# Optimization experiments

Measured on AMD Instinct MI355X. Metric: run time of the kernel, lower is better.

Reference implementation:

```python
import jax, jax.numpy as jnp
import numpy as np

Q_HEADS, KV_HEADS, D_K, D_V = 16, 4, 128, 128
GROUPS = Q_HEADS // KV_HEADS


def setup_inputs() -> dict:
    key = jax.random.key(0)
    ks = jax.random.split(key, 7)
    b, s, d = 2, 2048, 2048
    scale = 1.0 / np.sqrt(d).astype(np.float32)
    return {
        "Q": jax.random.normal(ks[0], (b, s, d), jnp.float32),
        "K": jax.random.normal(ks[1], (b, s, d), jnp.float32),
        "V": jax.random.normal(ks[2], (b, s, d), jnp.float32),
        "Wq": jax.random.normal(ks[3], (d, D_K * Q_HEADS), jnp.float32) * scale,
        "Wk": jax.random.normal(ks[4], (d, D_K * KV_HEADS), jnp.float32) * scale,
        "Wv": jax.random.normal(ks[5], (d, D_V * KV_HEADS), jnp.float32) * scale,
        "Wo": jax.random.normal(ks[6], (D_V * KV_HEADS, d), jnp.float32) * scale,
    }


def reference(Q, K, V, Wq, Wk, Wv, Wo):
    b, lq, _ = Q.shape
    lk = K.shape[1]
    # projections -> (b, heads, len, d)
    q = (Q @ Wq).reshape(b, lq, Q_HEADS, D_K).transpose(0, 2, 1, 3)
    k = (K @ Wk).reshape(b, lk, KV_HEADS, D_K).transpose(0, 2, 1, 3)
    v = (V @ Wv).reshape(b, lk, KV_HEADS, D_V).transpose(0, 2, 1, 3)
    # GQA quirk: scores summed over group dim g before softmax
    qr = q.reshape(b, GROUPS, KV_HEADS, lq, D_K)
    scores = jnp.einsum('bghqd,bhkd->bhqk', qr, k) / jnp.asarray(D_K ** 0.5, q.dtype)
    causal = jnp.tril(jnp.ones((lq, lk), bool))
    scores = jnp.where(causal[None, None], scores, jnp.asarray(-1e9, scores.dtype))
    attn = jax.nn.softmax(scores, axis=-1)  # (b, kv_heads, lq, lk)
    out = jnp.einsum('bhqk,bhkd->bhqd', attn, v)  # (b, kv_heads, lq, d_v)
    out = out.transpose(0, 2, 1, 3).reshape(b, lq, KV_HEADS * D_V)
    return out @ Wo
```

## Files before the change

### kernel.cpp

```cpp
#include <hip/hip_runtime.h>
#include <hip/hip_bf16.h>

typedef __attribute__((ext_vector_type(8))) short short8;
typedef __attribute__((ext_vector_type(4))) float f32x4;

#define MFMA16 __builtin_amdgcn_mfma_f32_16x16x32_bf16

__device__ inline unsigned short f2bf(float f) {
  __hip_bfloat16 h = __float2bfloat16(f);
  unsigned short u;
  __builtin_memcpy(&u, &h, 2);
  return u;
}

__device__ inline float bf2f(unsigned short u) {
  unsigned int x = ((unsigned int)u) << 16;
  float f;
  __builtin_memcpy(&f, &x, 4);
  return f;
}

__device__ inline void storeC(unsigned short* p, float v) { *p = f2bf(v); }
__device__ inline void storeC(float* p, float v) { *p = v; }

__device__ inline void gload16(const void* g, void* l) {
  __builtin_amdgcn_global_load_lds(
      (const __attribute__((address_space(1))) unsigned int*)g,
      (__attribute__((address_space(3))) unsigned int*)l,
      16, 0, 0);
}

__global__ __launch_bounds__(256)
void wqsum_t(const float* __restrict__ wq, unsigned short* __restrict__ dst) {
  __shared__ float t[64][65];
  const int n0 = blockIdx.x * 64, d0 = blockIdx.y * 64;
  const int tid = threadIdx.x;
#pragma unroll
  for (int it = 0; it < 16; ++it) {
    const int idx = it * 256 + tid;
    const int dd = idx >> 6, nn = idx & 63;
    const float* p = wq + (size_t)(d0 + dd) * 2048 + n0 + nn;
    t[dd][nn] = p[0] + p[512] + p[1024] + p[1536];
  }
  __syncthreads();
#pragma unroll
  for (int it = 0; it < 16; ++it) {
    const int idx = it * 256 + tid;
    const int nn = idx >> 6, dd = idx & 63;
    dst[(size_t)(n0 + nn) * 2048 + d0 + dd] = f2bf(t[dd][nn]);
  }
}

__global__ __launch_bounds__(256)
void transpose_w(const float* __restrict__ src, unsigned short* __restrict__ dst,
                 int R, int C) {
  __shared__ float t[64][65];
  const int c0 = blockIdx.x * 64, r0 = blockIdx.y * 64;
  const int tid = threadIdx.x;
#pragma unroll
  for (int it = 0; it < 16; ++it) {
    const int idx = it * 256 + tid;
    const int r = idx >> 6, c = idx & 63;
    t[r][c] = src[(size_t)(r0 + r) * C + c0 + c];
  }
  __syncthreads();
#pragma unroll
  for (int it = 0; it < 16; ++it) {
    const int idx = it * 256 + tid;
    const int rr = idx >> 6, cc = idx & 63;
    dst[(size_t)(c0 + rr) * R + r0 + cc] = f2bf(t[cc][rr]);
  }
}

__global__ __launch_bounds__(256)
void vtrans(const unsigned short* __restrict__ vh, unsigned short* __restrict__ vt) {
  __shared__ unsigned short t[64][72];
  const int s0 = blockIdx.x * 64;
  const int d0 = blockIdx.y * 64;
  const int bh = blockIdx.z;
  const int brow = (bh >> 2) * 2048;
  const int h = bh & 3;
  const int tid = threadIdx.x;
#pragma unroll
  for (int it = 0; it < 2; ++it) {
    const int idx = it * 256 + tid;
    const int s = idx >> 3;
    const int dd = (idx & 7) << 3;
    *(short8*)&t[s][dd] =
        *(const short8*)(vh + (size_t)(brow + s0 + s) * 512 + h * 128 + d0 + dd);
  }
  __syncthreads();
#pragma unroll
  for (int it = 0; it < 2; ++it) {
    const int idx = it * 256 + tid;
    const int dd = idx >> 3;
    const int ss = (idx & 7) << 3;
    short8 o;
#pragma unroll
    for (int e = 0; e < 8; ++e) o[e] = (short)t[ss + e][dd];
    *(short8*)(vt + ((size_t)bh * 128 + d0 + dd) * 2048 + s0 + ss) = o;
  }
}

template <bool AF32, typename CT, int KS>
__global__ __launch_bounds__(256)
void gemm_bt(const void* A0, const void* A1, const void* A2,
             const unsigned short* __restrict__ Bt, CT* __restrict__ C,
             int K, int N, size_t sB, size_t sC) {
  __shared__ unsigned short As[128 * 64];
  __shared__ unsigned short Bs[128 * 64];

  const int tid = threadIdx.x;
  const int lane = tid & 63;
  const int wv = tid >> 6;
  const int wm = (wv >> 1) << 6;
  const int wn = (wv & 1) << 6;
  const int l15 = lane & 15;
  const int l4 = lane >> 4;
  const int lsw = (l15 & 7) << 4;

  const int nwg = gridDim.x;
  const int bid = blockIdx.x;
  const int job = (bid & 7) * (nwg >> 3) + (bid >> 3);
  const int ntile = N >> 7;
  const int per_ks = nwg / KS;
  const int ks = (KS > 1) ? (job / per_ks) : 0;
  const int jj = job - ks * per_ks;
  const int z = jj / (32 * ntile);
  const int rem = jj - z * 32 * ntile;
  const int m0 = (rem / ntile) << 7;
  const int n0 = (rem % ntile) << 7;
  const int kbeg = ks * (K / KS);
  const int kend = kbeg + K / KS;

  const void* Az = (z == 0) ? A0 : (z == 1) ? A1 : A2;
  const unsigned short* Ab = (const unsigned short*)Az;
  const float* Af = (const float*)Az;
  const unsigned short* Bz = Bt + sB * (size_t)z;

  const f32x4 zero = {0.f, 0.f, 0.f, 0.f};
  f32x4 acc[4][4];
#pragma unroll
  for (int i = 0; i < 4; ++i)
#pragma unroll
    for (int j = 0; j < 4; ++j) acc[i][j] = zero;

  const int srow = tid >> 3;
  const int scol = (tid & 7) << 3;
  const int scolsw = scol ^ ((srow & 7) << 3);

  float4 ar[8];

  auto issueB = [&](int k0) {
#pragma unroll
    for (int s = 0; s < 4; ++s) {
      const unsigned short* bsrc =
          Bz + (size_t)(n0 + srow + s * 32) * K + k0 + scolsw;
      gload16(bsrc, (char*)Bs + tid * 16 + s * 4096);
    }
  };
  auto issueA16 = [&](int k0) {
#pragma unroll
    for (int s = 0; s < 4; ++s) {
      const unsigned short* asrc =
          Ab + (size_t)(m0 + srow + s * 32) * K + k0 + scolsw;
      gload16(asrc, (char*)As + tid * 16 + s * 4096);
    }
  };
  auto loadA = [&](int k0) {
#pragma unroll
    for (int s = 0; s < 4; ++s) {
      const float* asrc = Af + (size_t)(m0 + srow + s * 32) * K + k0 + scol;
      ar[2 * s] = *(const float4*)(asrc);
      ar[2 * s + 1] = *(const float4*)(asrc + 4);
    }
  };
  auto writeA = [&]() {
#pragma unroll
    for (int s = 0; s < 4; ++s) {
      short8 o;
      o[0] = (short)f2bf(ar[2 * s].x); o[1] = (short)f2bf(ar[2 * s].y);
      o[2] = (short)f2bf(ar[2 * s].z); o[3] = (short)f2bf(ar[2 * s].w);
      o[4] = (short)f2bf(ar[2 * s + 1].x); o[5] = (short)f2bf(ar[2 * s + 1].y);
      o[6] = (short)f2bf(ar[2 * s + 1].z); o[7] = (short)f2bf(ar[2 * s + 1].w);
      *(short8*)((char*)As + (srow + s * 32) * 128 + scolsw * 2) = o;
    }
  };

  if constexpr (AF32) loadA(kbeg);

  for (int k0 = kbeg; k0 < kend; k0 += 64) {
    if constexpr (AF32) writeA(); else issueA16(k0);
    issueB(k0);
    if constexpr (AF32) {
      if (k0 + 64 < kend) loadA(k0 + 64);
    }
    __syncthreads();
#pragma unroll
    for (int kk = 0; kk < 2; ++kk) {
      const int kb = (kk * 64 + (l4 << 4)) ^ lsw;
      short8 a[4], b[4];
#pragma unroll
      for (int i = 0; i < 4; ++i)
        a[i] = *(const short8*)((const char*)As + (wm + i * 16 + l15) * 128 + kb);
#pragma unroll
      for (int j = 0; j < 4; ++j)
        b[j] = *(const short8*)((const char*)Bs + (wn + j * 16 + l15) * 128 + kb);
#pragma unroll
      for (int i = 0; i < 4; ++i)
#pragma unroll
        for (int j = 0; j < 4; ++j)
          acc[i][j] = MFMA16(a[i], b[j], acc[i][j], 0, 0, 0);
    }
    __syncthreads();
  }

  CT* Cz = C + sC * (size_t)(ks * 3 + z);
#pragma unroll
  for (int i = 0; i < 4; ++i) {
    const int row0 = m0 + wm + i * 16 + (l4 << 2);
#pragma unroll
    for (int j = 0; j < 4; ++j) {
      const int col = n0 + wn + j * 16 + l15;
#pragma unroll
      for (int r = 0; r < 4; ++r)
        storeC(&Cz[(size_t)(row0 + r) * N + col], acc[i][j][r]);
    }
  }
}

__global__ __launch_bounds__(256)
void qkv_combine(const unsigned short* __restrict__ pC,
                 unsigned short* __restrict__ dst) {
  const size_t HALF = 6291456;
  size_t i = ((size_t)blockIdx.x * 256 + threadIdx.x) * 8;
  const size_t stride = (size_t)gridDim.x * 256 * 8;
  for (; i < HALF; i += stride) {
    const short8 a = *(const short8*)(pC + i);
    const short8 b = *(const short8*)(pC + HALF + i);
    short8 o;
#pragma unroll
    for (int e = 0; e < 8; ++e)
      o[e] = (short)f2bf(bf2f((unsigned short)a[e]) + bf2f((unsigned short)b[e]));
    *(short8*)(dst + i) = o;
  }
}

__global__ __launch_bounds__(128)
void attn_split(const unsigned short* __restrict__ qh,
                const unsigned short* __restrict__ kh,
                const unsigned short* __restrict__ vt,
                unsigned short* __restrict__ Oh,
                unsigned short* __restrict__ pO,
                float* __restrict__ pml) {
  __shared__ unsigned short P_lds[2][32][36];
  const int tid = threadIdx.x;
  const int lane = tid & 63;
  const int wave = tid >> 6;
  const int l15 = lane & 15;
  const int l4 = lane >> 4;
  const int bh = blockIdx.y;
  const int brow = (bh >> 2) * 2048;
  const int h = bh & 3;

  int j = blockIdx.x, g = 0;
  while (j >= 2 * (g + 1) * (g + 2)) ++g;
  const int rem = j - 2 * g * (g + 1);
  const int r_ = rem / (g + 1);
  const int c_ = rem - r_ * (g + 1);
  const int qt = 4 * g + r_;
  const int k_begin = c_ << 8;
  const int k_end = (c_ == g) ? (qt + 1) * 64 : ((c_ + 1) << 8);
  const int qrow_w = qt * 64 + wave * 32;
  const float SCALE = 0.08838834764831845f;

  short8 qf[2][4];
#pragma unroll
  for (int m = 0; m < 2; ++m) {
    const unsigned short* qp =
        qh + (size_t)(brow + qrow_w + m * 16 + l15) * 512 + h * 128 + (l4 << 3);
#pragma unroll
    for (int kk = 0; kk < 4; ++kk) qf[m][kk] = *(const short8*)(qp + kk * 32);
  }

  const f32x4 zero = {0.f, 0.f, 0.f, 0.f};
  f32x4 o_acc[2][8];
#pragma unroll
  for (int m = 0; m < 2; ++m)
#pragma unroll
    for (int i = 0; i < 8; ++i) o_acc[m][i] = zero;
  float m_run[2][4], l_run[2][4];
#pragma unroll
  for (int m = 0; m < 2; ++m)
#pragma unroll
    for (int r = 0; r < 4; ++r) { m_run[m][r] = -1e30f; l_run[m][r] = 0.f; }

  const int nt = (k_end - k_begin) >> 5;
  for (int t = 0; t < nt; ++t) {
    const int kbase = k_begin + t * 32;
    f32x4 sa[2][2];
    sa[0][0] = zero; sa[0][1] = zero; sa[1][0] = zero; sa[1][1] = zero;
#pragma unroll
    for (int n = 0; n < 2; ++n) {
      short8 kf[4];
      const unsigned short* kp =
          kh + (size_t)(brow + kbase + n * 16 + l15) * 512 + h * 128 + (l4 << 3);
#pragma unroll
      for (int kk = 0; kk < 4; ++kk) kf[kk] = *(const short8*)(kp + kk * 32);
#pragma unroll
      for (int kk = 0; kk < 4; ++kk) {
        sa[0][n] = MFMA16(qf[0][kk], kf[kk], sa[0][n], 0, 0, 0);
        sa[1][n] = MFMA16(qf[1][kk], kf[kk], sa[1][n], 0, 0, 0);
      }
    }
    const bool need_mask = (kbase + 31 > qrow_w);
    float p[2][2][4];
#pragma unroll
    for (int m = 0; m < 2; ++m)
#pragma unroll
      for (int n = 0; n < 2; ++n)
#pragma unroll
        for (int r = 0; r < 4; ++r) {
          float v = sa[m][n][r] * SCALE;
          if (need_mask) {
            const int kc = kbase + n * 16 + l15;
            const int qr = qrow_w + m * 16 + (l4 << 2) + r;
            if (kc > qr) v = -1e30f;
          }
          p[m][n][r] = v;
        }
    float alpha[2][4];
#pragma unroll
    for (int m = 0; m < 2; ++m)
#pragma unroll
      for (int r = 0; r < 4; ++r) {
        float tmax = fmaxf(p[m][0][r], p[m][1][r]);
#pragma unroll
        for (int o = 1; o <= 8; o <<= 1) tmax = fmaxf(tmax, __shfl_xor(tmax, o));
        const float mn = fmaxf(m_run[m][r], tmax);
        alpha[m][r] = __expf(m_run[m][r] - mn);
        m_run[m][r] = mn;
      }
#pragma unroll
    for (int m = 0; m < 2; ++m)
#pragma unroll
      for (int r = 0; r < 4; ++r) {
        p[m][0][r] = __expf(p[m][0][r] - m_run[m][r]);
        p[m][1][r] = __expf(p[m][1][r] - m_run[m][r]);
        float s = p[m][0][r] + p[m][1][r];
#pragma unroll
        for (int o = 1; o <= 8; o <<= 1) s += __shfl_xor(s, o);
        l_run[m][r] = l_run[m][r] * alpha[m][r] + s;
      }
#pragma unroll
    for (int m = 0; m < 2; ++m)
#pragma unroll
      for (int d8 = 0; d8 < 8; ++d8)
#pragma unroll
        for (int r = 0; r < 4; ++r) o_acc[m][d8][r] *= alpha[m][r];
#pragma unroll
    for (int m = 0; m < 2; ++m)
#pragma unroll
      for (int n = 0; n < 2; ++n)
#pragma unroll
        for (int r = 0; r < 4; ++r)
          P_lds[wave][m * 16 + (l4 << 2) + r][n * 16 + l15] = f2bf(p[m][n][r]);
    short8 pa[2];
#pragma unroll
    for (int m = 0; m < 2; ++m)
      pa[m] = *(const short8*)((const char*)&P_lds[wave][0][0] +
                               (m * 16 + l15) * 72 + (l4 << 4));
#pragma unroll
    for (int d8 = 0; d8 < 8; ++d8) {
      const short8 vb = *(const short8*)(
          vt + ((size_t)bh * 128 + d8 * 16 + l15) * 2048 + kbase + (l4 << 3));
      o_acc[0][d8] = MFMA16(pa[0], vb, o_acc[0][d8], 0, 0, 0);
      o_acc[1][d8] = MFMA16(pa[1], vb, o_acc[1][d8], 0, 0, 0);
    }
  }

  if (g == 0) {
#pragma unroll
    for (int m = 0; m < 2; ++m)
#pragma unroll
      for (int d8 = 0; d8 < 8; ++d8)
#pragma unroll
        for (int r = 0; r < 4; ++r) {
          const int row = brow + qrow_w + m * 16 + (l4 << 2) + r;
          Oh[(size_t)row * 512 + h * 128 + d8 * 16 + l15] =
              f2bf(o_acc[m][d8][r] / l_run[m][r]);
        }
  } else {
    const int slot = bh * 144 + blockIdx.x;
    unsigned short* po = pO + (size_t)slot * 64 * 128;
#pragma unroll
    for (int m = 0; m < 2; ++m)
#pragma unroll
      for (int d8 = 0; d8 < 8; ++d8)
#pragma unroll
        for (int r = 0; r < 4; ++r) {
          const int row = wave * 32 + m * 16 + (l4 << 2) + r;
          po[row * 128 + d8 * 16 + l15] = f2bf(o_acc[m][d8][r]);
        }
    if (l15 == 0) {
#pragma unroll
      for (int m = 0; m < 2; ++m)
#pragma unroll
        for (int r = 0; r < 4; ++r) {
          const int row = wave * 32 + m * 16 + (l4 << 2) + r;
          pml[((size_t)slot * 64 + row) * 2 + 0] = m_run[m][r];
          pml[((size_t)slot * 64 + row) * 2 + 1] = l_run[m][r];
        }
    }
  }
}

__global__ __launch_bounds__(256)
void attn_combine(const unsigned short* __restrict__ pO,
                  const float* __restrict__ pml,
                  unsigned short* __restrict__ Oh) {
  const int bh = blockIdx.y;
  const int qt = 4 + blockIdx.x;
  const int g = qt >> 2;
  const int nch = g + 1;
  const int base = 2 * g * (g + 1) + (qt & 3) * (g + 1);
  const int slot0 = bh * 144 + base;
  const int brow = (bh >> 2) * 2048;
  const int h = bh & 3;
#pragma unroll
  for (int u = 0; u < 4; ++u) {
    const int unit = u * 256 + threadIdx.x;
    const int row = unit >> 4;
    const int c8 = (unit & 15) << 3;
    float M = -1e30f;
    for (int c = 0; c < nch; ++c)
      M = fmaxf(M, pml[((size_t)(slot0 + c) * 64 + row) * 2]);
    float L = 0.f;
    float acc[8] = {0.f, 0.f, 0.f, 0.f, 0.f, 0.f, 0.f, 0.f};
    for (int c = 0; c < nch; ++c) {
      const float mc = pml[((size_t)(slot0 + c) * 64 + row) * 2];
      const float lc = pml[((size_t)(slot0 + c) * 64 + row) * 2 + 1];
      const float w = __expf(mc - M);
      L += w * lc;
      const short8 ov =
          *(const short8*)(pO + ((size_t)(slot0 + c) * 64 + row) * 128 + c8);
#pragma unroll
      for (int e = 0; e < 8; ++e) acc[e] += w * bf2f((unsigned short)ov[e]);
    }
    const float inv = 1.f / L;
    short8 o;
#pragma unroll
    for (int e = 0; e < 8; ++e) o[e] = (short)f2bf(acc[e] * inv);
    *(short8*)(Oh + (size_t)(brow + qt * 64 + row) * 512 + h * 128 + c8) = o;
  }
}

extern "C" void kernel_launch(void* const* d_in, const int* in_sizes, int n_in,
                              void* d_out, int out_size, void* d_ws, size_t ws_size,
                              hipStream_t stream) {
  const float* Q  = (const float*)d_in[0];
  const float* K_ = (const float*)d_in[1];
  const float* V  = (const float*)d_in[2];
  const float* Wq = (const float*)d_in[3];
  const float* Wk = (const float*)d_in[4];
  const float* Wv = (const float*)d_in[5];
  const float* Wo = (const float*)d_in[6];
  float* out = (float*)d_out;

  char* ws = (char*)d_ws;
  unsigned short* Wt  = (unsigned short*)ws;
  unsigned short* WoT = (unsigned short*)(ws + 6291456);
  unsigned short* qh  = (unsigned short*)(ws + 8388608);
  unsigned short* kh  = qh + 2097152;
  unsigned short* vh  = qh + 2 * 2097152;
  unsigned short* Oh  = qh + 3 * 2097152;
  unsigned short* vt  = (unsigned short*)(ws + 25165824);
  unsigned short* pO  = (unsigned short*)(ws + 29360128);
  float*          pml = (float*)(ws + 48234496);
  unsigned short* pC  = (unsigned short*)(ws + 20971520);

  wqsum_t<<<dim3(8, 32), 256, 0, stream>>>(Wq, Wt);
  transpose_w<<<dim3(8, 32), 256, 0, stream>>>(Wk, Wt + 1048576, 2048, 512);
  transpose_w<<<dim3(8, 32), 256, 0, stream>>>(Wv, Wt + 2097152, 2048, 512);
  transpose_w<<<dim3(32, 8), 256, 0, stream>>>(Wo, WoT, 512, 2048);

  gemm_bt<true, unsigned short, 2><<<768, 256, 0, stream>>>(
      Q, K_, V, Wt, pC, 2048, 512, 1048576, 2097152);
  qkv_combine<<<1024, 256, 0, stream>>>(pC, qh);

  vtrans<<<dim3(32, 2, 8), 256, 0, stream>>>(vh, vt);

  attn_split<<<dim3(144, 8), 128, 0, stream>>>(qh, kh, vt, Oh, pO, pml);
  attn_combine<<<dim3(28, 8), 256, 0, stream>>>(pO, pml, Oh);

  gemm_bt<false, float, 1><<<512, 256, 0, stream>>>(
      Oh, Oh, Oh, WoT, out, 512, 2048, 0, 0);
}
```

Measured before the change: 157.7 us.

## Stage K/V tiles in double-buffered LDS with 128-row query blocks

The attention kernel now uses 4 waves covering 128 query rows per block. K and V tiles are loaded cooperatively into swizzled, double-buffered shared memory, so all waves reuse them instead of each wave reading global memory on its own. The softmax switches to exp2 with the log2e folded into the scale, and it skips the rescale of the running max when the new max stays within a threshold. The split/combine tiling is reworked for the larger query tile. In exchange the block needs more shared memory and a barrier every tile, fewer blocks are launched, and waves above the diagonal sit idle inside causal tiles.

```diff
diff --git a/kernel.cpp b/kernel.cpp
--- a/kernel.cpp
+++ b/kernel.cpp
@@ -246,14 +246,17 @@
   }
 }
 
-__global__ __launch_bounds__(128)
+__global__ __launch_bounds__(256)
 void attn_split(const unsigned short* __restrict__ qh,
                 const unsigned short* __restrict__ kh,
                 const unsigned short* __restrict__ vt,
                 unsigned short* __restrict__ Oh,
                 unsigned short* __restrict__ pO,
                 float* __restrict__ pml) {
-  __shared__ unsigned short P_lds[2][32][36];
+  __shared__ unsigned short K_lds[2][32 * 128];
+  __shared__ unsigned short V_lds[2][128 * 32];
+  __shared__ unsigned short P_lds[4][32][36];
+
   const int tid = threadIdx.x;
   const int lane = tid & 63;
   const int wave = tid >> 6;
@@ -263,16 +266,16 @@
   const int brow = (bh >> 2) * 2048;
   const int h = bh & 3;
 
-  int j = blockIdx.x, g = 0;
-  while (j >= 2 * (g + 1) * (g + 2)) ++g;
-  const int rem = j - 2 * g * (g + 1);
-  const int r_ = rem / (g + 1);
-  const int c_ = rem - r_ * (g + 1);
-  const int qt = 4 * g + r_;
+  int j = blockIdx.x;
+  int qt = 0;
+  while (j >= (qt >> 1) + 1) { j -= (qt >> 1) + 1; ++qt; }
+  const int c_ = j;
+  const int nch = (qt >> 1) + 1;
   const int k_begin = c_ << 8;
-  const int k_end = (c_ == g) ? (qt + 1) * 64 : ((c_ + 1) << 8);
-  const int qrow_w = qt * 64 + wave * 32;
-  const float SCALE = 0.08838834764831845f;
+  const int cend = (c_ + 1) << 8, qend = (qt + 1) << 7;
+  const int k_end = cend < qend ? cend : qend;
+  const int qrow_w = (qt << 7) + (wave << 5);
+  const float SCALE2 = 0.127517424f;
 
   short8 qf[2][4];
 #pragma unroll
@@ -295,91 +298,136 @@
 #pragma unroll
     for (int r = 0; r < 4; ++r) { m_run[m][r] = -1e30f; l_run[m][r] = 0.f; }
 
+  auto stageK = [&](int buf, int kbase) {
+#pragma unroll
+    for (int i = 0; i < 2; ++i) {
+      const int flat = i * 4096 + tid * 16;
+      const int r = flat >> 8;
+      const int scoff = (flat & 255) ^ ((r & 7) << 4);
+      const char* src = (const char*)kh +
+          ((size_t)(brow + kbase + r) * 512 + h * 128) * 2 + scoff;
+      gload16(src, (char*)&K_lds[buf][0] + flat);
+    }
+  };
+  auto stageV = [&](int buf, int kbase) {
+#pragma unroll
+    for (int i = 0; i < 2; ++i) {
+      const int flat = i * 4096 + tid * 16;
+      const int d = flat >> 6;
+      const int scoff = (flat & 63) ^ ((d & 3) << 4);
+      const char* src = (const char*)vt +
+          ((size_t)((size_t)bh * 128 + d) * 2048 + kbase) * 2 + scoff;
+      gload16(src, (char*)&V_lds[buf][0] + flat);
+    }
+  };
+
   const int nt = (k_end - k_begin) >> 5;
+  stageK(0, k_begin);
+  stageV(0, k_begin);
+  __syncthreads();
+
+  int cur = 0;
   for (int t = 0; t < nt; ++t) {
     const int kbase = k_begin + t * 32;
-    f32x4 sa[2][2];
-    sa[0][0] = zero; sa[0][1] = zero; sa[1][0] = zero; sa[1][1] = zero;
-#pragma unroll
-    for (int n = 0; n < 2; ++n) {
-      short8 kf[4];
-      const unsigned short* kp =
-          kh + (size_t)(brow + kbase + n * 16 + l15) * 512 + h * 128 + (l4 << 3);
-#pragma unroll
-      for (int kk = 0; kk < 4; ++kk) kf[kk] = *(const short8*)(kp + kk * 32);
-#pragma unroll
-      for (int kk = 0; kk < 4; ++kk) {
-        sa[0][n] = MFMA16(qf[0][kk], kf[kk], sa[0][n], 0, 0, 0);
-        sa[1][n] = MFMA16(qf[1][kk], kf[kk], sa[1][n], 0, 0, 0);
+    if (t + 1 < nt) {
+      stageK(cur ^ 1, kbase + 32);
+      stageV(cur ^ 1, kbase + 32);
+    }
+    if (kbase <= qrow_w + 31) {
+      f32x4 sa[2][2];
+      sa[0][0] = zero; sa[0][1] = zero; sa[1][0] = zero; sa[1][1] = zero;
+#pragma unroll
+      for (int n = 0; n < 2; ++n) {
+        const int row = n * 16 + l15;
+        const int swz = (row & 7) << 4;
+#pragma unroll
+        for (int kk = 0; kk < 4; ++kk) {
+          const short8 kf = *(const short8*)((const char*)&K_lds[cur][0] +
+                              row * 256 + ((kk * 64 + (l4 << 4)) ^ swz));
+          sa[0][n] = MFMA16(qf[0][kk], kf, sa[0][n], 0, 0, 0);
+          sa[1][n] = MFMA16(qf[1][kk], kf, sa[1][n], 0, 0, 0);
+        }
       }
-    }
-    const bool need_mask = (kbase + 31 > qrow_w);
-    float p[2][2][4];
-#pragma unroll
-    for (int m = 0; m < 2; ++m)
-#pragma unroll
-      for (int n = 0; n < 2; ++n)
+      const bool need_mask = (kbase + 31 > qrow_w);
+      float p[2][2][4];
+#pragma unroll
+      for (int m = 0; m < 2; ++m)
+#pragma unroll
+        for (int n = 0; n < 2; ++n)
+#pragma unroll
+          for (int r = 0; r < 4; ++r) {
+            float v = sa[m][n][r] * SCALE2;
+            if (need_mask) {
+              const int kc = kbase + n * 16 + l15;
+              const int qr = qrow_w + m * 16 + (l4 << 2) + r;
+              if (kc > qr) v = -1e30f;
+            }
+            p[m][n][r] = v;
+          }
+      float pmax[2][4];
+#pragma unroll
+      for (int m = 0; m < 2; ++m)
 #pragma unroll
         for (int r = 0; r < 4; ++r) {
-          float v = sa[m][n][r] * SCALE;
-          if (need_mask) {
-            const int kc = kbase + n * 16 + l15;
-            const int qr = qrow_w + m * 16 + (l4 << 2) + r;
-            if (kc > qr) v = -1e30f;
+          float tmax = fmaxf(p[m][0][r], p[m][1][r]);
+#pragma unroll
+          for (int o = 1; o <= 8; o <<= 1) tmax = fmaxf(tmax, __shfl_xor(tmax, o));
+          pmax[m][r] = tmax;
+        }
+#pragma unroll
+      for (int m = 0; m < 2; ++m) {
+        bool near = true;
+#pragma unroll
+        for (int r = 0; r < 4; ++r) near = near && (pmax[m][r] <= m_run[m][r] + 8.f);
+        if (!__all(near)) {
+#pragma unroll
+          for (int r = 0; r < 4; ++r) {
+            const float mn = fmaxf(m_run[m][r], pmax[m][r]);
+            const float alpha = exp2f(m_run[m][r] - mn);
+            m_run[m][r] = mn;
+            l_run[m][r] *= alpha;
+#pragma unroll
+            for (int d8 = 0; d8 < 8; ++d8) o_acc[m][d8][r] *= alpha;
           }
-          p[m][n][r] = v;
-        }
-    float alpha[2][4];
-#pragma unroll
-    for (int m = 0; m < 2; ++m)
-#pragma unroll
-      for (int r = 0; r < 4; ++r) {
-        float tmax = fmaxf(p[m][0][r], p[m][1][r]);
-#pragma unroll
-        for (int o = 1; o <= 8; o <<= 1) tmax = fmaxf(tmax, __shfl_xor(tmax, o));
-        const float mn = fmaxf(m_run[m][r], tmax);
-        alpha[m][r] = __expf(m_run[m][r] - mn);
-        m_run[m][r] = mn;
+        }
       }
 #pragma unroll
-    for (int m = 0; m < 2; ++m)
-#pragma unroll
-      for (int r = 0; r < 4; ++r) {
-        p[m][0][r] = __expf(p[m][0][r] - m_run[m][r]);
-        p[m][1][r] = __expf(p[m][1][r] - m_run[m][r]);
-        float s = p[m][0][r] + p[m][1][r];
-#pragma unroll
-        for (int o = 1; o <= 8; o <<= 1) s += __shfl_xor(s, o);
-        l_run[m][r] = l_run[m][r] * alpha[m][r] + s;
+      for (int m = 0; m < 2; ++m)
+#pragma unroll
+        for (int r = 0; r < 4; ++r) {
+          p[m][0][r] = exp2f(p[m][0][r] - m_run[m][r]);
+          p[m][1][r] = exp2f(p[m][1][r] - m_run[m][r]);
+          float s = p[m][0][r] + p[m][1][r];
+#pragma unroll
+          for (int o = 1; o <= 8; o <<= 1) s += __shfl_xor(s, o);
+          l_run[m][r] += s;
+        }
+#pragma unroll
+      for (int m = 0; m < 2; ++m)
+#pragma unroll
+        for (int n = 0; n < 2; ++n)
+#pragma unroll
+          for (int r = 0; r < 4; ++r)
+            P_lds[wave][m * 16 + (l4 << 2) + r][n * 16 + l15] = f2bf(p[m][n][r]);
+      short8 pa[2];
+#pragma unroll
+      for (int m = 0; m < 2; ++m)
+        pa[m] = *(const short8*)((const char*)&P_lds[wave][0][0] +
+                                 (m * 16 + l15) * 72 + (l4 << 4));
+#pragma unroll
+      for (int d8 = 0; d8 < 8; ++d8) {
+        const int row = d8 * 16 + l15;
+        const short8 vb = *(const short8*)((const char*)&V_lds[cur][0] +
+                            row * 64 + ((l4 << 4) ^ ((row & 3) << 4)));
+        o_acc[0][d8] = MFMA16(pa[0], vb, o_acc[0][d8], 0, 0, 0);
+        o_acc[1][d8] = MFMA16(pa[1], vb, o_acc[1][d8], 0, 0, 0);
       }
-#pragma unroll
-    for (int m = 0; m < 2; ++m)
-#pragma unroll
-      for (int d8 = 0; d8 < 8; ++d8)
-#pragma unroll
-        for (int r = 0; r < 4; ++r) o_acc[m][d8][r] *= alpha[m][r];
-#pragma unroll
-    for (int m = 0; m < 2; ++m)
-#pragma unroll
-      for (int n = 0; n < 2; ++n)
-#pragma unroll
-        for (int r = 0; r < 4; ++r)
-          P_lds[wave][m * 16 + (l4 << 2) + r][n * 16 + l15] = f2bf(p[m][n][r]);
-    short8 pa[2];
-#pragma unroll
-    for (int m = 0; m < 2; ++m)
-      pa[m] = *(const short8*)((const char*)&P_lds[wave][0][0] +
-                               (m * 16 + l15) * 72 + (l4 << 4));
-#pragma unroll
-    for (int d8 = 0; d8 < 8; ++d8) {
-      const short8 vb = *(const short8*)(
-          vt + ((size_t)bh * 128 + d8 * 16 + l15) * 2048 + kbase + (l4 << 3));
-      o_acc[0][d8] = MFMA16(pa[0], vb, o_acc[0][d8], 0, 0, 0);
-      o_acc[1][d8] = MFMA16(pa[1], vb, o_acc[1][d8], 0, 0, 0);
-    }
-  }
-
-  if (g == 0) {
+    }
+    __syncthreads();
+    cur ^= 1;
+  }
+
+  if (nch == 1) {
 #pragma unroll
     for (int m = 0; m < 2; ++m)
 #pragma unroll
@@ -391,15 +439,15 @@
               f2bf(o_acc[m][d8][r] / l_run[m][r]);
         }
   } else {
-    const int slot = bh * 144 + blockIdx.x;
-    unsigned short* po = pO + (size_t)slot * 64 * 128;
+    const int slot = bh * 72 + blockIdx.x;
+    unsigned short* po = pO + (size_t)slot * 128 * 128;
 #pragma unroll
     for (int m = 0; m < 2; ++m)
 #pragma unroll
       for (int d8 = 0; d8 < 8; ++d8)
 #pragma unroll
         for (int r = 0; r < 4; ++r) {
-          const int row = wave * 32 + m * 16 + (l4 << 2) + r;
+          const int row = (wave << 5) + m * 16 + (l4 << 2) + r;
           po[row * 128 + d8 * 16 + l15] = f2bf(o_acc[m][d8][r]);
         }
     if (l15 == 0) {
@@ -407,9 +455,9 @@
       for (int m = 0; m < 2; ++m)
 #pragma unroll
         for (int r = 0; r < 4; ++r) {
-          const int row = wave * 32 + m * 16 + (l4 << 2) + r;
-          pml[((size_t)slot * 64 + row) * 2 + 0] = m_run[m][r];
-          pml[((size_t)slot * 64 + row) * 2 + 1] = l_run[m][r];
+          const int row = (wave << 5) + m * 16 + (l4 << 2) + r;
+          pml[((size_t)slot * 128 + row) * 2 + 0] = m_run[m][r];
+          pml[((size_t)slot * 128 + row) * 2 + 1] = l_run[m][r];
         }
     }
   }
@@ -420,30 +468,30 @@
                   const float* __restrict__ pml,
                   unsigned short* __restrict__ Oh) {
   const int bh = blockIdx.y;
-  const int qt = 4 + blockIdx.x;
-  const int g = qt >> 2;
-  const int nch = g + 1;
-  const int base = 2 * g * (g + 1) + (qt & 3) * (g + 1);
-  const int slot0 = bh * 144 + base;
+  const int qt = 2 + blockIdx.x;
+  const int a = qt >> 1;
+  const int nch = a + 1;
+  const int base = a * a + a + ((qt & 1) ? (a + 1) : 0);
+  const int slot0 = bh * 72 + base;
   const int brow = (bh >> 2) * 2048;
   const int h = bh & 3;
 #pragma unroll
-  for (int u = 0; u < 4; ++u) {
+  for (int u = 0; u < 8; ++u) {
     const int unit = u * 256 + threadIdx.x;
     const int row = unit >> 4;
     const int c8 = (unit & 15) << 3;
     float M = -1e30f;
     for (int c = 0; c < nch; ++c)
-      M = fmaxf(M, pml[((size_t)(slot0 + c) * 64 + row) * 2]);
+      M = fmaxf(M, pml[((size_t)(slot0 + c) * 128 + row) * 2]);
     float L = 0.f;
     float acc[8] = {0.f, 0.f, 0.f, 0.f, 0.f, 0.f, 0.f, 0.f};
     for (int c = 0; c < nch; ++c) {
-      const float mc = pml[((size_t)(slot0 + c) * 64 + row) * 2];
-      const float lc = pml[((size_t)(slot0 + c) * 64 + row) * 2 + 1];
-      const float w = __expf(mc - M);
+      const float mc = pml[((size_t)(slot0 + c) * 128 + row) * 2];
+      const float lc = pml[((size_t)(slot0 + c) * 128 + row) * 2 + 1];
+      const float w = exp2f(mc - M);
       L += w * lc;
       const short8 ov =
-          *(const short8*)(pO + ((size_t)(slot0 + c) * 64 + row) * 128 + c8);
+          *(const short8*)(pO + ((size_t)(slot0 + c) * 128 + row) * 128 + c8);
 #pragma unroll
       for (int e = 0; e < 8; ++e) acc[e] += w * bf2f((unsigned short)ov[e]);
     }
@@ -451,7 +499,7 @@
     short8 o;
 #pragma unroll
     for (int e = 0; e < 8; ++e) o[e] = (short)f2bf(acc[e] * inv);
-    *(short8*)(Oh + (size_t)(brow + qt * 64 + row) * 512 + h * 128 + c8) = o;
+    *(short8*)(Oh + (size_t)(brow + (qt << 7) + row) * 512 + h * 128 + c8) = o;
   }
 }
 
@@ -490,8 +538,8 @@
 
   vtrans<<<dim3(32, 2, 8), 256, 0, stream>>>(vh, vt);
 
-  attn_split<<<dim3(144, 8), 128, 0, stream>>>(qh, kh, vt, Oh, pO, pml);
-  attn_combine<<<dim3(28, 8), 256, 0, stream>>>(pO, pml, Oh);
+  attn_split<<<dim3(72, 8), 256, 0, stream>>>(qh, kh, vt, Oh, pO, pml);
+  attn_combine<<<dim3(14, 8), 256, 0, stream>>>(pO, pml, Oh);
 
   gemm_bt<false, float, 1><<<512, 256, 0, stream>>>(
       Oh, Oh, Oh, WoT, out, 512, 2048, 0, 0);
```

After: 188.2 us. 19.4% more time.

## Use exp2 softmax with lazy rescaling, MFMA row sums, and interleaved head grid

Applied to the files above, without the earlier changes.

The attention split kernel now folds log2(e) into the score scale so it can use exp2f. It rescales the running max and accumulators only when a new tile max exceeds the old max by more than 8. Row sums are accumulated with an MFMA against a ones vector instead of shuffle reductions, and fully masked key tiles per wave are skipped. The grid is flattened so the 8 batch-heads are interleaved with work chunks, changing the dispatch order. Together these aim to cut exp, shuffle and rescale ALU work in the inner loop and balance the causal workload, at the cost of one extra MFMA pair per tile and a bounded growth of unnormalized values.

```diff
diff --git a/kernel.cpp b/kernel.cpp
--- a/kernel.cpp
+++ b/kernel.cpp
@@ -259,11 +259,12 @@
   const int wave = tid >> 6;
   const int l15 = lane & 15;
   const int l4 = lane >> 4;
-  const int bh = blockIdx.y;
+  const int bh = blockIdx.x & 7;
+  const int jid = blockIdx.x >> 3;
   const int brow = (bh >> 2) * 2048;
   const int h = bh & 3;
 
-  int j = blockIdx.x, g = 0;
+  int j = jid, g = 0;
   while (j >= 2 * (g + 1) * (g + 2)) ++g;
   const int rem = j - 2 * g * (g + 1);
   const int r_ = rem / (g + 1);
@@ -272,7 +273,7 @@
   const int k_begin = c_ << 8;
   const int k_end = (c_ == g) ? (qt + 1) * 64 : ((c_ + 1) << 8);
   const int qrow_w = qt * 64 + wave * 32;
-  const float SCALE = 0.08838834764831845f;
+  const float SCALE2 = 0.127517424f;
 
   short8 qf[2][4];
 #pragma unroll
@@ -283,21 +284,29 @@
     for (int kk = 0; kk < 4; ++kk) qf[m][kk] = *(const short8*)(qp + kk * 32);
   }
 
+  short8 oneb;
+#pragma unroll
+  for (int e = 0; e < 8; ++e) oneb[e] = (short)0x3F80;
+
   const f32x4 zero = {0.f, 0.f, 0.f, 0.f};
   f32x4 o_acc[2][8];
+  f32x4 l_acc[2];
+#pragma unroll
+  for (int m = 0; m < 2; ++m) {
+    l_acc[m] = zero;
+#pragma unroll
+    for (int i = 0; i < 8; ++i) o_acc[m][i] = zero;
+  }
+  float m_run[2][4];
 #pragma unroll
   for (int m = 0; m < 2; ++m)
 #pragma unroll
-    for (int i = 0; i < 8; ++i) o_acc[m][i] = zero;
-  float m_run[2][4], l_run[2][4];
-#pragma unroll
-  for (int m = 0; m < 2; ++m)
-#pragma unroll
-    for (int r = 0; r < 4; ++r) { m_run[m][r] = -1e30f; l_run[m][r] = 0.f; }
+    for (int r = 0; r < 4; ++r) m_run[m][r] = -1e30f;
 
   const int nt = (k_end - k_begin) >> 5;
   for (int t = 0; t < nt; ++t) {
     const int kbase = k_begin + t * 32;
+    if (kbase > qrow_w + 31) continue;
     f32x4 sa[2][2];
     sa[0][0] = zero; sa[0][1] = zero; sa[1][0] = zero; sa[1][1] = zero;
 #pragma unroll
@@ -321,7 +330,7 @@
       for (int n = 0; n < 2; ++n)
 #pragma unroll
         for (int r = 0; r < 4; ++r) {
-          float v = sa[m][n][r] * SCALE;
+          float v = sa[m][n][r] * SCALE2;
           if (need_mask) {
             const int kc = kbase + n * 16 + l15;
             const int qr = qrow_w + m * 16 + (l4 << 2) + r;
@@ -329,7 +338,7 @@
           }
           p[m][n][r] = v;
         }
-    float alpha[2][4];
+    float pmax[2][4];
 #pragma unroll
     for (int m = 0; m < 2; ++m)
 #pragma unroll
@@ -337,27 +346,32 @@
         float tmax = fmaxf(p[m][0][r], p[m][1][r]);
 #pragma unroll
         for (int o = 1; o <= 8; o <<= 1) tmax = fmaxf(tmax, __shfl_xor(tmax, o));
-        const float mn = fmaxf(m_run[m][r], tmax);
-        alpha[m][r] = __expf(m_run[m][r] - mn);
-        m_run[m][r] = mn;
+        pmax[m][r] = tmax;
       }
 #pragma unroll
-    for (int m = 0; m < 2; ++m)
-#pragma unroll
-      for (int r = 0; r < 4; ++r) {
-        p[m][0][r] = __expf(p[m][0][r] - m_run[m][r]);
-        p[m][1][r] = __expf(p[m][1][r] - m_run[m][r]);
-        float s = p[m][0][r] + p[m][1][r];
-#pragma unroll
-        for (int o = 1; o <= 8; o <<= 1) s += __shfl_xor(s, o);
-        l_run[m][r] = l_run[m][r] * alpha[m][r] + s;
+    for (int m = 0; m < 2; ++m) {
+      bool near = true;
+#pragma unroll
+      for (int r = 0; r < 4; ++r) near = near && (pmax[m][r] <= m_run[m][r] + 8.f);
+      if (!__all(near)) {
+#pragma unroll
+        for (int r = 0; r < 4; ++r) {
+          const float mn = fmaxf(m_run[m][r], pmax[m][r]);
+          const float alpha = exp2f(m_run[m][r] - mn);
+          m_run[m][r] = mn;
+          l_acc[m][r] *= alpha;
+#pragma unroll
+          for (int d8 = 0; d8 < 8; ++d8) o_acc[m][d8][r] *= alpha;
+        }
       }
-#pragma unroll
-    for (int m = 0; m < 2; ++m)
-#pragma unroll
-      for (int d8 = 0; d8 < 8; ++d8)
-#pragma unroll
-        for (int r = 0; r < 4; ++r) o_acc[m][d8][r] *= alpha[m][r];
+    }
+#pragma unroll
+    for (int m = 0; m < 2; ++m)
+#pragma unroll
+      for (int n = 0; n < 2; ++n)
+#pragma unroll
+        for (int r = 0; r < 4; ++r)
+          p[m][n][r] = exp2f(p[m][n][r] - m_run[m][r]);
 #pragma unroll
     for (int m = 0; m < 2; ++m)
 #pragma unroll
@@ -370,6 +384,8 @@
     for (int m = 0; m < 2; ++m)
       pa[m] = *(const short8*)((const char*)&P_lds[wave][0][0] +
                                (m * 16 + l15) * 72 + (l4 << 4));
+    l_acc[0] = MFMA16(pa[0], oneb, l_acc[0], 0, 0, 0);
+    l_acc[1] = MFMA16(pa[1], oneb, l_acc[1], 0, 0, 0);
 #pragma unroll
     for (int d8 = 0; d8 < 8; ++d8) {
       const short8 vb = *(const short8*)(
@@ -388,10 +404,10 @@
         for (int r = 0; r < 4; ++r) {
           const int row = brow + qrow_w + m * 16 + (l4 << 2) + r;
           Oh[(size_t)row * 512 + h * 128 + d8 * 16 + l15] =
-              f2bf(o_acc[m][d8][r] / l_run[m][r]);
+              f2bf(o_acc[m][d8][r] / l_acc[m][r]);
         }
   } else {
-    const int slot = bh * 144 + blockIdx.x;
+    const int slot = bh * 144 + jid;
     unsigned short* po = pO + (size_t)slot * 64 * 128;
 #pragma unroll
     for (int m = 0; m < 2; ++m)
@@ -409,7 +425,7 @@
         for (int r = 0; r < 4; ++r) {
           const int row = wave * 32 + m * 16 + (l4 << 2) + r;
           pml[((size_t)slot * 64 + row) * 2 + 0] = m_run[m][r];
-          pml[((size_t)slot * 64 + row) * 2 + 1] = l_run[m][r];
+          pml[((size_t)slot * 64 + row) * 2 + 1] = l_acc[m][r];
         }
     }
   }
@@ -440,7 +456,7 @@
     for (int c = 0; c < nch; ++c) {
       const float mc = pml[((size_t)(slot0 + c) * 64 + row) * 2];
       const float lc = pml[((size_t)(slot0 + c) * 64 + row) * 2 + 1];
-      const float w = __expf(mc - M);
+      const float w = exp2f(mc - M);
       L += w * lc;
       const short8 ov =
           *(const short8*)(pO + ((size_t)(slot0 + c) * 64 + row) * 128 + c8);
@@ -490,7 +506,7 @@
 
   vtrans<<<dim3(32, 2, 8), 256, 0, stream>>>(vh, vt);
 
-  attn_split<<<dim3(144, 8), 128, 0, stream>>>(qh, kh, vt, Oh, pO, pml);
+  attn_split<<<1152, 128, 0, stream>>>(qh, kh, vt, Oh, pO, pml);
   attn_combine<<<dim3(28, 8), 256, 0, stream>>>(pO, pml, Oh);
 
   gemm_bt<false, float, 1><<<512, 256, 0, stream>>>(
```

New measurement: 155.3 us. About the same (-1.5%).
